# Kernel optimization log

Measured on AMD Instinct MI355X. Metric: run time of the kernel, lower is better.

Reference implementation:

```python
import jax, jax.numpy as jnp
import numpy as np

NEG_SLOPE = 0.2

def setup_inputs() -> dict:
    key = jax.random.key(0)
    k1, k2, k3, k4, k5 = jax.random.split(key, 5)
    N_src, N_dst, E, H, D = 50000, 50000, 1600000, 8, 16
    return {
        "h_src": jax.random.normal(k1, (N_src, H * D), dtype=jnp.float32),
        "h_dst": jax.random.normal(k2, (N_dst, H * D), dtype=jnp.float32),
        "attn_l": jax.random.normal(k3, (1, H, D), dtype=jnp.float32),
        "src": jax.random.randint(k4, (E,), 0, N_src, dtype=jnp.int32),
        "dst": jax.random.randint(k5, (E,), 0, N_dst, dtype=jnp.int32),
    }

def reference(h_src, h_dst, attn_l, src, dst):
    N_dst = h_dst.shape[0]
    H, D = attn_l.shape[1], attn_l.shape[2]
    hs = h_src.reshape(-1, H, D)                       # [N_src, H, D]
    el = jnp.sum(hs * attn_l, axis=-1)                 # [N_src, H] per-node attn logit
    e = jax.nn.leaky_relu(el[src], NEG_SLOPE)          # [E, H] per-edge score
    # edge softmax over incoming edges of each dst node (stable)
    seg_max = jax.ops.segment_max(e, dst, num_segments=N_dst)   # [N_dst, H]
    ex = jnp.exp(e - seg_max[dst])                     # [E, H]
    denom = jax.ops.segment_sum(ex, dst, num_segments=N_dst)    # [N_dst, H]
    a = ex / denom[dst]                                # [E, H]
    # gather-multiply-scatter: u_mul_e then sum by dst
    m = hs[src] * a[:, :, None]                        # [E, H, D]
    out = jax.ops.segment_sum(m, dst, num_segments=N_dst)       # [N_dst, H, D]
    return out.reshape(N_dst, H * D)
```

## Files before the change

kernel.cpp:

```cpp
#include <hip/hip_runtime.h>

#define Hh 8
#define HD 128
#define NEG_SLOPE 0.2f
#define EPB 4096


__device__ __forceinline__ unsigned bfr(float f) {
    unsigned u = __float_as_uint(f);
    return (u + 0x7fffu + ((u >> 16) & 1u)) >> 16;
}
__device__ __forceinline__ unsigned pk(float a, float b) { return bfr(a) | (bfr(b) << 16); }

__global__ void __launch_bounds__(1024)
k_b1(const int* __restrict__ dst, int* __restrict__ gh,
     int E, int nblk, int nbkt,
     const float* __restrict__ hs, const float* __restrict__ attn,
     float* __restrict__ ew, uint4* __restrict__ hsb, int nh_src) {
    int t = threadIdx.x;
    if ((int)blockIdx.x < nblk) {
        __shared__ int lh[256];
        if (t < 256) lh[t] = 0;
        __syncthreads();
        int base = blockIdx.x * EPB;
        int cnt = E - base; if (cnt > EPB) cnt = EPB;
        int i = t * 4;
        if (i + 3 < cnt) {
            int4 d = *(const int4*)(dst + base + i);
            atomicAdd(&lh[d.x >> 8], 1);
            atomicAdd(&lh[d.y >> 8], 1);
            atomicAdd(&lh[d.z >> 8], 1);
            atomicAdd(&lh[d.w >> 8], 1);
        } else {
            for (int e = i; e < cnt; ++e) atomicAdd(&lh[dst[base + e] >> 8], 1);
        }
        __syncthreads();
        if (t < nbkt) gh[t * nblk + blockIdx.x] = lh[t];
    } else {
        int i = ((int)blockIdx.x - nblk) * 1024 + t;
        if (i >= nh_src) return;
        int n = i >> 3, h = i & 7;
        const float4* a = (const float4*)(hs + (size_t)n * HD + h * 16);
        const float4* w = (const float4*)(attn + h * 16);
        float4 x0 = a[0], x1 = a[1], x2 = a[2], x3 = a[3];
        float4 w0 = w[0], w1 = w[1], w2 = w[2], w3 = w[3];
        float s = x0.x * w0.x + x0.y * w0.y + x0.z * w0.z + x0.w * w0.w
                + x1.x * w1.x + x1.y * w1.y + x1.z * w1.z + x1.w * w1.w
                + x2.x * w2.x + x2.y * w2.y + x2.z * w2.z + x2.w * w2.w
                + x3.x * w3.x + x3.y * w3.y + x3.z * w3.z + x3.w * w3.w;
        s = (s >= 0.f) ? s : NEG_SLOPE * s;
        ew[i] = __expf(s);
        uint4 p0 = { pk(x0.x, x0.y), pk(x0.z, x0.w), pk(x1.x, x1.y), pk(x1.z, x1.w) };
        uint4 p1 = { pk(x2.x, x2.y), pk(x2.z, x2.w), pk(x3.x, x3.y), pk(x3.z, x3.w) };
        hsb[(size_t)n * 16 + h * 2]     = p0;
        hsb[(size_t)n * 16 + h * 2 + 1] = p1;
    }
}

__global__ void k_gsum(const int* __restrict__ g, int* __restrict__ partial, int n) {
    __shared__ int sh[256];
    int t = threadIdx.x;
    int i = blockIdx.x * 256 + t;
    sh[t] = (i < n) ? g[i] : 0;
    __syncthreads();
    for (int off = 128; off > 0; off >>= 1) {
        if (t < off) sh[t] += sh[t + off];
        __syncthreads();
    }
    if (t == 0) partial[blockIdx.x] = sh[0];
}

__global__ void k_gscan(int* __restrict__ g, const int* __restrict__ partial, int n) {
    __shared__ int sh[256];
    __shared__ int pre_s;
    int t = threadIdx.x;
    int acc = 0;
    for (int k = t; k < (int)blockIdx.x; k += 256) acc += partial[k];
    sh[t] = acc;
    __syncthreads();
    for (int off = 128; off > 0; off >>= 1) {
        if (t < off) sh[t] += sh[t + off];
        __syncthreads();
    }
    if (t == 0) pre_s = sh[0];
    __syncthreads();
    int pre = pre_s;
    int i = blockIdx.x * 256 + t;
    int v = (i < n) ? g[i] : 0;
    __syncthreads();
    sh[t] = v;
    __syncthreads();
    for (int off = 1; off < 256; off <<= 1) {
        int x = (t >= off) ? sh[t - off] : 0;
        __syncthreads();
        sh[t] += x;
        __syncthreads();
    }
    if (i < n) g[i] = pre + sh[t] - v;
}

__global__ void __launch_bounds__(1024)
k_b2(const int* __restrict__ src, const int* __restrict__ dst,
     const int* __restrict__ gh, int* __restrict__ tmp,
     int E, int nblk, int nbkt) {
    __shared__ int cur[256];
    int t = threadIdx.x, blk = blockIdx.x;
    if (t < nbkt) cur[t] = gh[t * nblk + blk];
    __syncthreads();
    int base = blk * EPB;
    int cnt = E - base; if (cnt > EPB) cnt = EPB;
    int i = t * 4;
    if (i + 3 < cnt) {
        int4 d = *(const int4*)(dst + base + i);
        int4 s = *(const int4*)(src + base + i);
        int p;
        p = atomicAdd(&cur[d.x >> 8], 1); tmp[p] = ((d.x & 255) << 16) | s.x;
        p = atomicAdd(&cur[d.y >> 8], 1); tmp[p] = ((d.y & 255) << 16) | s.y;
        p = atomicAdd(&cur[d.z >> 8], 1); tmp[p] = ((d.z & 255) << 16) | s.z;
        p = atomicAdd(&cur[d.w >> 8], 1); tmp[p] = ((d.w & 255) << 16) | s.w;
    } else {
        for (int e = i; e < cnt; ++e) {
            int d = dst[base + e];
            int p = atomicAdd(&cur[d >> 8], 1);
            tmp[p] = ((d & 255) << 16) | src[base + e];
        }
    }
}

__global__ void __launch_bounds__(1024)
k_b3(const int* __restrict__ gh, const int* __restrict__ tmp,
     unsigned short* __restrict__ adj, int* __restrict__ row_ptr,
     int E, int nblk, int nbkt, int ndst) {
    __shared__ int lh[256], sh[256], cur[256];
    int b = blockIdx.x, t = threadIdx.x;
    int s0 = gh[b * nblk];
    int s1 = (b + 1 < nbkt) ? gh[(b + 1) * nblk] : E;
    if (t < 256) lh[t] = 0;
    __syncthreads();
    for (int j = s0 + t; j < s1; j += 1024)
        atomicAdd(&lh[tmp[j] >> 16], 1);
    __syncthreads();
    int v = 0;
    if (t < 256) { v = lh[t]; sh[t] = v; }
    __syncthreads();
    for (int off = 1; off < 256; off <<= 1) {
        int x = 0;
        if (t < 256 && t >= off) x = sh[t - off];
        __syncthreads();
        if (t < 256) sh[t] += x;
        __syncthreads();
    }
    if (t < 256) {
        int start = s0 + sh[t] - v;
        cur[t] = start;
        int d = b * 256 + t;
        if (d < ndst) row_ptr[d] = start;
        if (b == nbkt - 1 && t == 0) row_ptr[ndst] = E;
    }
    __syncthreads();
    for (int j = s0 + t; j < s1; j += 1024) {
        int w = tmp[j];
        int pos = atomicAdd(&cur[w >> 16], 1);
        adj[pos] = (unsigned short)(w & 0xffff);
    }
}

#define ACC8(X, W) \
    a0.x += __uint_as_float((X).x << 16) * (W); \
    a0.y += __uint_as_float((X).x & 0xffff0000u) * (W); \
    a0.z += __uint_as_float((X).y << 16) * (W); \
    a0.w += __uint_as_float((X).y & 0xffff0000u) * (W); \
    a1.x += __uint_as_float((X).z << 16) * (W); \
    a1.y += __uint_as_float((X).z & 0xffff0000u) * (W); \
    a1.z += __uint_as_float((X).w << 16) * (W); \
    a1.w += __uint_as_float((X).w & 0xffff0000u) * (W);

__global__ void __launch_bounds__(128)
k_agg(const int* __restrict__ row_ptr, const unsigned short* __restrict__ adj,
      const uint4* __restrict__ hsb, const float* __restrict__ ew,
      float* __restrict__ out) {
    int d = blockIdx.x;
    int t = threadIdx.x;
    int j0 = row_ptr[d], j1 = row_ptr[d + 1];
    int q = t & 15;
    int slot = t >> 4;
    int h = q >> 1;

    float4 a0 = {0.f, 0.f, 0.f, 0.f}, a1 = {0.f, 0.f, 0.f, 0.f};
    float ws = 0.f;
    int j = j0 + slot;
    for (; j + 24 < j1; j += 32) {
        int s0 = adj[j], s1 = adj[j + 8], s2 = adj[j + 16], s3 = adj[j + 24];
        float w0 = ew[s0 * Hh + h], w1 = ew[s1 * Hh + h];
        float w2 = ew[s2 * Hh + h], w3 = ew[s3 * Hh + h];
        uint4 x0 = hsb[(size_t)s0 * 16 + q];
        uint4 x1 = hsb[(size_t)s1 * 16 + q];
        uint4 x2 = hsb[(size_t)s2 * 16 + q];
        uint4 x3 = hsb[(size_t)s3 * 16 + q];
        ACC8(x0, w0)
        ACC8(x1, w1)
        ACC8(x2, w2)
        ACC8(x3, w3)
        ws += w0 + w1 + w2 + w3;
    }
    for (; j < j1; j += 8) {
        int s0 = adj[j];
        float w0 = ew[s0 * Hh + h];
        uint4 x0 = hsb[(size_t)s0 * 16 + q];
        ACC8(x0, w0)
        ws += w0;
    }

#pragma unroll
    for (int off = 16; off <= 32; off <<= 1) {
        a0.x += __shfl_xor(a0.x, off, 64);
        a0.y += __shfl_xor(a0.y, off, 64);
        a0.z += __shfl_xor(a0.z, off, 64);
        a0.w += __shfl_xor(a0.w, off, 64);
        a1.x += __shfl_xor(a1.x, off, 64);
        a1.y += __shfl_xor(a1.y, off, 64);
        a1.z += __shfl_xor(a1.z, off, 64);
        a1.w += __shfl_xor(a1.w, off, 64);
        ws   += __shfl_xor(ws,   off, 64);
    }
    __shared__ float4 sp0[16], sp1[16];
    __shared__ float wsp[16];
    if (t >= 64 && t < 80) { sp0[q] = a0; sp1[q] = a1; wsp[q] = ws; }
    __syncthreads();
    if (t < 16) {
        float wt = ws + wsp[t];
        float r = (wt > 0.f) ? 1.0f / wt : 0.f;
        float4 o0 = sp0[t], o1 = sp1[t];
        o0.x = (a0.x + o0.x) * r; o0.y = (a0.y + o0.y) * r;
        o0.z = (a0.z + o0.z) * r; o0.w = (a0.w + o0.w) * r;
        o1.x = (a1.x + o1.x) * r; o1.y = (a1.y + o1.y) * r;
        o1.z = (a1.z + o1.z) * r; o1.w = (a1.w + o1.w) * r;
        float4* op = (float4*)(out + (size_t)d * HD + t * 8);
        op[0] = o0;
        op[1] = o1;
    }
}

extern "C" void kernel_launch(void* const* d_in, const int* in_sizes, int n_in,
                              void* d_out, int out_size, void* d_ws, size_t ws_size,
                              hipStream_t stream) {
    const float* h_src  = (const float*)d_in[0];
    const float* attn_l = (const float*)d_in[2];
    const int*   src    = (const int*)d_in[3];
    const int*   dst    = (const int*)d_in[4];
    float* out = (float*)d_out;

    const int N_src = in_sizes[0] / HD;
    const int N_dst = in_sizes[1] / HD;
    const int E     = in_sizes[3];
    const int NH_src = N_src * Hh;

    const int NBLK = (E + EPB - 1) / EPB;
    const int NBKT = (N_dst + 255) / 256;
    const int M    = NBKT * NBLK;
    const int NC   = (M + 255) / 256;
    const int NB_EW = (NH_src + 1023) / 1024;

    unsigned short* hsb = (unsigned short*)d_ws;
    float* ew      = (float*)(hsb + (size_t)N_src * HD);
    int*   tmp     = (int*)(ew + NH_src);
    unsigned short* adj = (unsigned short*)(tmp + E);
    int*   gh      = (int*)(adj + (((size_t)E + 1) & ~(size_t)1));
    int*   partial = gh + M;
    int*   row_ptr = partial + NC;

    k_b1<<<NBLK + NB_EW, 1024, 0, stream>>>(dst, gh, E, NBLK, NBKT,
                                            h_src, attn_l, ew, (uint4*)hsb, NH_src);
    k_gsum <<<NC, 256, 0, stream>>>(gh, partial, M);
    k_gscan<<<NC, 256, 0, stream>>>(gh, partial, M);
    k_b2<<<NBLK, 1024, 0, stream>>>(src, dst, gh, tmp, E, NBLK, NBKT);
    k_b3<<<NBKT, 1024, 0, stream>>>(gh, tmp, adj, row_ptr, E, NBLK, NBKT, N_dst);
    k_agg<<<N_dst, 128, 0, stream>>>(row_ptr, adj, (const uint4*)hsb, ew, out);
}
```

Before: 194.5 us.

## Replace scan-based bucket sort with fixed-capacity buckets filled via global atomics

```diff
diff --git a/kernel.cpp b/kernel.cpp
--- a/kernel.cpp
+++ b/kernel.cpp
@@ -4,6 +4,7 @@
 #define HD 128
 #define NEG_SLOPE 0.2f
 #define EPB 4096
+#define CAP 12288
 
 
 __device__ __forceinline__ unsigned bfr(float f) {
@@ -13,20 +14,24 @@
 __device__ __forceinline__ unsigned pk(float a, float b) { return bfr(a) | (bfr(b) << 16); }
 
 __global__ void __launch_bounds__(1024)
-k_b1(const int* __restrict__ dst, int* __restrict__ gh,
-     int E, int nblk, int nbkt,
-     const float* __restrict__ hs, const float* __restrict__ attn,
-     float* __restrict__ ew, uint4* __restrict__ hsb, int nh_src) {
+k_sort(const int* __restrict__ src, const int* __restrict__ dst,
+       unsigned* __restrict__ tmp, int* __restrict__ blen,
+       int E, int nblk, int nbkt,
+       const float* __restrict__ hs, const float* __restrict__ attn,
+       float* __restrict__ ew, uint4* __restrict__ hsb, int nh_src) {
     int t = threadIdx.x;
     if ((int)blockIdx.x < nblk) {
-        __shared__ int lh[256];
+        __shared__ int lh[256], cur[256];
         if (t < 256) lh[t] = 0;
         __syncthreads();
         int base = blockIdx.x * EPB;
         int cnt = E - base; if (cnt > EPB) cnt = EPB;
         int i = t * 4;
-        if (i + 3 < cnt) {
-            int4 d = *(const int4*)(dst + base + i);
+        int4 d, s;
+        bool vec = (i + 3 < cnt);
+        if (vec) {
+            d = *(const int4*)(dst + base + i);
+            s = *(const int4*)(src + base + i);
             atomicAdd(&lh[d.x >> 8], 1);
             atomicAdd(&lh[d.y >> 8], 1);
             atomicAdd(&lh[d.z >> 8], 1);
@@ -35,7 +40,29 @@
             for (int e = i; e < cnt; ++e) atomicAdd(&lh[dst[base + e] >> 8], 1);
         }
         __syncthreads();
-        if (t < nbkt) gh[t * nblk + blockIdx.x] = lh[t];
+        if (t < 256) {
+            int v = lh[t];
+            cur[t] = atomicAdd(&blen[t * 16], v);
+        }
+        __syncthreads();
+        if (vec) {
+            int p;
+            p = atomicAdd(&cur[d.x >> 8], 1);
+            tmp[(size_t)(d.x >> 8) * CAP + p] = ((unsigned)(d.x & 255) << 16) | (unsigned)s.x;
+            p = atomicAdd(&cur[d.y >> 8], 1);
+            tmp[(size_t)(d.y >> 8) * CAP + p] = ((unsigned)(d.y & 255) << 16) | (unsigned)s.y;
+            p = atomicAdd(&cur[d.z >> 8], 1);
+            tmp[(size_t)(d.z >> 8) * CAP + p] = ((unsigned)(d.z & 255) << 16) | (unsigned)s.z;
+            p = atomicAdd(&cur[d.w >> 8], 1);
+            tmp[(size_t)(d.w >> 8) * CAP + p] = ((unsigned)(d.w & 255) << 16) | (unsigned)s.w;
+        } else {
+            for (int e = i; e < cnt; ++e) {
+                int dd = dst[base + e];
+                int p = atomicAdd(&cur[dd >> 8], 1);
+                tmp[(size_t)(dd >> 8) * CAP + p] =
+                    ((unsigned)(dd & 255) << 16) | (unsigned)src[base + e];
+            }
+        }
     } else {
         int i = ((int)blockIdx.x - nblk) * 1024 + t;
         if (i >= nh_src) return;
@@ -44,12 +71,12 @@
         const float4* w = (const float4*)(attn + h * 16);
         float4 x0 = a[0], x1 = a[1], x2 = a[2], x3 = a[3];
         float4 w0 = w[0], w1 = w[1], w2 = w[2], w3 = w[3];
-        float s = x0.x * w0.x + x0.y * w0.y + x0.z * w0.z + x0.w * w0.w
-                + x1.x * w1.x + x1.y * w1.y + x1.z * w1.z + x1.w * w1.w
-                + x2.x * w2.x + x2.y * w2.y + x2.z * w2.z + x2.w * w2.w
-                + x3.x * w3.x + x3.y * w3.y + x3.z * w3.z + x3.w * w3.w;
-        s = (s >= 0.f) ? s : NEG_SLOPE * s;
-        ew[i] = __expf(s);
+        float sv = x0.x * w0.x + x0.y * w0.y + x0.z * w0.z + x0.w * w0.w
+                 + x1.x * w1.x + x1.y * w1.y + x1.z * w1.z + x1.w * w1.w
+                 + x2.x * w2.x + x2.y * w2.y + x2.z * w2.z + x2.w * w2.w
+                 + x3.x * w3.x + x3.y * w3.y + x3.z * w3.z + x3.w * w3.w;
+        sv = (sv >= 0.f) ? sv : NEG_SLOPE * sv;
+        ew[i] = __expf(sv);
         uint4 p0 = { pk(x0.x, x0.y), pk(x0.z, x0.w), pk(x1.x, x1.y), pk(x1.z, x1.w) };
         uint4 p1 = { pk(x2.x, x2.y), pk(x2.z, x2.w), pk(x3.x, x3.y), pk(x3.z, x3.w) };
         hsb[(size_t)n * 16 + h * 2]     = p0;
@@ -57,91 +84,21 @@
     }
 }
 
-__global__ void k_gsum(const int* __restrict__ g, int* __restrict__ partial, int n) {
-    __shared__ int sh[256];
-    int t = threadIdx.x;
-    int i = blockIdx.x * 256 + t;
-    sh[t] = (i < n) ? g[i] : 0;
-    __syncthreads();
-    for (int off = 128; off > 0; off >>= 1) {
-        if (t < off) sh[t] += sh[t + off];
-        __syncthreads();
-    }
-    if (t == 0) partial[blockIdx.x] = sh[0];
-}
-
-__global__ void k_gscan(int* __restrict__ g, const int* __restrict__ partial, int n) {
-    __shared__ int sh[256];
-    __shared__ int pre_s;
-    int t = threadIdx.x;
-    int acc = 0;
-    for (int k = t; k < (int)blockIdx.x; k += 256) acc += partial[k];
-    sh[t] = acc;
-    __syncthreads();
-    for (int off = 128; off > 0; off >>= 1) {
-        if (t < off) sh[t] += sh[t + off];
-        __syncthreads();
-    }
-    if (t == 0) pre_s = sh[0];
-    __syncthreads();
-    int pre = pre_s;
-    int i = blockIdx.x * 256 + t;
-    int v = (i < n) ? g[i] : 0;
-    __syncthreads();
-    sh[t] = v;
-    __syncthreads();
-    for (int off = 1; off < 256; off <<= 1) {
-        int x = (t >= off) ? sh[t - off] : 0;
-        __syncthreads();
-        sh[t] += x;
-        __syncthreads();
-    }
-    if (i < n) g[i] = pre + sh[t] - v;
-}
-
 __global__ void __launch_bounds__(1024)
-k_b2(const int* __restrict__ src, const int* __restrict__ dst,
-     const int* __restrict__ gh, int* __restrict__ tmp,
-     int E, int nblk, int nbkt) {
-    __shared__ int cur[256];
-    int t = threadIdx.x, blk = blockIdx.x;
-    if (t < nbkt) cur[t] = gh[t * nblk + blk];
-    __syncthreads();
-    int base = blk * EPB;
-    int cnt = E - base; if (cnt > EPB) cnt = EPB;
-    int i = t * 4;
-    if (i + 3 < cnt) {
-        int4 d = *(const int4*)(dst + base + i);
-        int4 s = *(const int4*)(src + base + i);
-        int p;
-        p = atomicAdd(&cur[d.x >> 8], 1); tmp[p] = ((d.x & 255) << 16) | s.x;
-        p = atomicAdd(&cur[d.y >> 8], 1); tmp[p] = ((d.y & 255) << 16) | s.y;
-        p = atomicAdd(&cur[d.z >> 8], 1); tmp[p] = ((d.z & 255) << 16) | s.z;
-        p = atomicAdd(&cur[d.w >> 8], 1); tmp[p] = ((d.w & 255) << 16) | s.w;
-    } else {
-        for (int e = i; e < cnt; ++e) {
-            int d = dst[base + e];
-            int p = atomicAdd(&cur[d >> 8], 1);
-            tmp[p] = ((d & 255) << 16) | src[base + e];
-        }
-    }
-}
-
-__global__ void __launch_bounds__(1024)
-k_b3(const int* __restrict__ gh, const int* __restrict__ tmp,
+k_b3(const unsigned* __restrict__ tmp, const int* __restrict__ blen,
      unsigned short* __restrict__ adj, int* __restrict__ row_ptr,
-     int E, int nblk, int nbkt, int ndst) {
+     int E, int nbkt, int ndst) {
+    __shared__ unsigned seg[CAP];
     __shared__ int lh[256], sh[256], cur[256];
+    __shared__ int base_s;
     int b = blockIdx.x, t = threadIdx.x;
-    int s0 = gh[b * nblk];
-    int s1 = (b + 1 < nbkt) ? gh[(b + 1) * nblk] : E;
-    if (t < 256) lh[t] = 0;
-    __syncthreads();
-    for (int j = s0 + t; j < s1; j += 1024)
-        atomicAdd(&lh[tmp[j] >> 16], 1);
-    __syncthreads();
-    int v = 0;
-    if (t < 256) { v = lh[t]; sh[t] = v; }
+    int nb = blen[b * 16];
+    int bc = 0;
+    if (t < 256) {
+        bc = (t < nbkt) ? blen[t * 16] : 0;
+        sh[t] = bc;
+        lh[t] = 0;
+    }
     __syncthreads();
     for (int off = 1; off < 256; off <<= 1) {
         int x = 0;
@@ -150,17 +107,37 @@
         if (t < 256) sh[t] += x;
         __syncthreads();
     }
+    if (t == b) base_s = sh[t] - bc;
+    __syncthreads();
+    int base_b = base_s;
+    const unsigned* tp = tmp + (size_t)b * CAP;
+    for (int j = t; j < nb; j += 1024) {
+        unsigned w = tp[j];
+        seg[j] = w;
+        atomicAdd(&lh[(w >> 16) & 255], 1);
+    }
+    __syncthreads();
+    int v = 0;
+    if (t < 256) { v = lh[t]; sh[t] = v; }
+    __syncthreads();
+    for (int off = 1; off < 256; off <<= 1) {
+        int x = 0;
+        if (t < 256 && t >= off) x = sh[t - off];
+        __syncthreads();
+        if (t < 256) sh[t] += x;
+        __syncthreads();
+    }
     if (t < 256) {
-        int start = s0 + sh[t] - v;
+        int start = base_b + sh[t] - v;
         cur[t] = start;
         int d = b * 256 + t;
         if (d < ndst) row_ptr[d] = start;
-        if (b == nbkt - 1 && t == 0) row_ptr[ndst] = E;
-    }
-    __syncthreads();
-    for (int j = s0 + t; j < s1; j += 1024) {
-        int w = tmp[j];
-        int pos = atomicAdd(&cur[w >> 16], 1);
+        if (b == 0 && t == 0) row_ptr[ndst] = E;
+    }
+    __syncthreads();
+    for (int j = t; j < nb; j += 1024) {
+        unsigned w = seg[j];
+        int pos = atomicAdd(&cur[(w >> 16) & 255], 1);
         adj[pos] = (unsigned short)(w & 0xffff);
     }
 }
@@ -255,25 +232,20 @@
     const int E     = in_sizes[3];
     const int NH_src = N_src * Hh;
 
-    const int NBLK = (E + EPB - 1) / EPB;
-    const int NBKT = (N_dst + 255) / 256;
-    const int M    = NBKT * NBLK;
-    const int NC   = (M + 255) / 256;
+    const int NBLK  = (E + EPB - 1) / EPB;
+    const int NBKT  = (N_dst + 255) / 256;
     const int NB_EW = (NH_src + 1023) / 1024;
 
     unsigned short* hsb = (unsigned short*)d_ws;
-    float* ew      = (float*)(hsb + (size_t)N_src * HD);
-    int*   tmp     = (int*)(ew + NH_src);
-    unsigned short* adj = (unsigned short*)(tmp + E);
-    int*   gh      = (int*)(adj + (((size_t)E + 1) & ~(size_t)1));
-    int*   partial = gh + M;
-    int*   row_ptr = partial + NC;
-
-    k_b1<<<NBLK + NB_EW, 1024, 0, stream>>>(dst, gh, E, NBLK, NBKT,
-                                            h_src, attn_l, ew, (uint4*)hsb, NH_src);
-    k_gsum <<<NC, 256, 0, stream>>>(gh, partial, M);
-    k_gscan<<<NC, 256, 0, stream>>>(gh, partial, M);
-    k_b2<<<NBLK, 1024, 0, stream>>>(src, dst, gh, tmp, E, NBLK, NBKT);
-    k_b3<<<NBKT, 1024, 0, stream>>>(gh, tmp, adj, row_ptr, E, NBLK, NBKT, N_dst);
+    float* ew = (float*)(hsb + (size_t)N_src * HD);
+    unsigned* tmp = (unsigned*)(ew + NH_src);
+    unsigned short* adj = (unsigned short*)(tmp + (size_t)NBKT * CAP);
+    int* blen    = (int*)(adj + (((size_t)E + 1) & ~(size_t)1));
+    int* row_ptr = blen + 256 * 16;
+
+    hipMemsetAsync(blen, 0, 256 * 16 * sizeof(int), stream);
+    k_sort<<<NBLK + NB_EW, 1024, 0, stream>>>(src, dst, tmp, blen, E, NBLK, NBKT,
+                                              h_src, attn_l, ew, (uint4*)hsb, NH_src);
+    k_b3<<<NBKT, 1024, 0, stream>>>(tmp, blen, adj, row_ptr, E, NBKT, N_dst);
     k_agg<<<N_dst, 128, 0, stream>>>(row_ptr, adj, (const uint4*)hsb, ew, out);
 }
```

Result: no change. 194.6 us (+0.0%).
